# Optimization experiments

Hardware: AMD Instinct MI355X
Metric: run time of the kernel (lower is better)

## Reference

```python
import jax, jax.numpy as jnp
import numpy as np

N_HEAD = 16

def _alibi_slopes(num_heads):
    # m_i = (256 ** (1/num_heads)) ** -(i+1)
    x = (2.0 ** 8) ** (1.0 / num_heads)
    return jnp.asarray([1.0 / x ** (i + 1) for i in range(num_heads)], dtype=jnp.float32)

def setup_inputs() -> dict:
    key = jax.random.key(0)
    k1, k2 = jax.random.split(key)
    B, S, D = 2, 2048, 1024
    x = jax.random.normal(k1, (B, S, D), dtype=jnp.float32)
    W_kqv = jax.random.normal(k2, (D, 3 * D), dtype=jnp.float32) * 0.02
    return {"x": x, "W_kqv": W_kqv}

def reference(x, W_kqv):
    B, S, D = x.shape
    H = N_HEAD
    hd = D // H
    scale = jnp.sqrt(jnp.asarray(D, dtype=x.dtype))  # NOTE: sqrt(n_embd), per source
    kqv = x @ W_kqv                                   # [B,S,3D]
    k, q, v = jnp.split(kqv, 3, axis=-1)              # chunk order: key, query, value
    q = q.reshape(B, S, H, hd).transpose(0, 2, 1, 3)  # [B,H,S,hd]
    k = k.reshape(B, S, H, hd).transpose(0, 2, 1, 3)
    v = v.reshape(B, S, H, hd).transpose(0, 2, 1, 3)
    # ALiBi bias: m[h] * (j - i)
    pos = jnp.arange(S)
    rel = (pos[None, :] - pos[:, None]).astype(x.dtype)      # [S,S]
    m = _alibi_slopes(H).astype(x.dtype)                     # [H]
    bias = m[:, None, None] * rel                            # [H,S,S]
    score = jnp.einsum('bhqd,bhkd->bhqk', q, k) / scale + bias[None]
    causal = pos[None, :] <= pos[:, None]                    # [S,S] lower-tri
    score = jnp.where(causal[None, None], score, -jnp.inf)
    attn = jax.nn.softmax(score, axis=-1)                    # [B,H,S,S]
    out = jnp.einsum('bhqk,bhkd->bhqd', attn, v)
    out = out.transpose(0, 2, 1, 3).reshape(B, S, D)
    return (out, attn)
```

## Files before the change

kernel.cpp:

```cpp
#include <hip/hip_runtime.h>
#include <hip/hip_bf16.h>

typedef __attribute__((ext_vector_type(8))) short short8;
typedef __attribute__((ext_vector_type(4))) float f32x4;

static __device__ __forceinline__ unsigned short f2bf(float f) {
    unsigned int x = __float_as_uint(f);
    x += 0x7fffu + ((x >> 16) & 1u);
    return (unsigned short)(x >> 16);
}

static __device__ __forceinline__ void gld_lds16(const unsigned short* g, unsigned short* l) {
    __builtin_amdgcn_global_load_lds((const __attribute__((address_space(1))) void*)g,
                                     (__attribute__((address_space(3))) void*)l, 16, 0, 0);
}

__global__ __launch_bounds__(256) void cvt_x_kernel(const float* __restrict__ in,
                                                    unsigned short* __restrict__ outb,
                                                    int n4) {
    int i = blockIdx.x * 256 + threadIdx.x;
    if (i < n4) {
        f32x4 v = *(const f32x4*)(in + (size_t)i * 4);
        ushort4 o;
        o.x = f2bf(v[0]); o.y = f2bf(v[1]); o.z = f2bf(v[2]); o.w = f2bf(v[3]);
        *(ushort4*)(outb + (size_t)i * 4) = o;
    }
}

__global__ __launch_bounds__(256) void cvt_wt_kernel(const float* __restrict__ W,
                                                     unsigned short* __restrict__ WT) {
    __shared__ float t[64][65];
    const int n0 = blockIdx.x * 64;
    const int k0 = blockIdx.y * 64;
    const int tid = threadIdx.x;
#pragma unroll
    for (int i = 0; i < 16; ++i) {
        int lin = tid + i * 256;
        int rr = lin >> 6, cc = lin & 63;
        t[rr][cc] = W[(size_t)(k0 + rr) * 3072 + n0 + cc];
    }
    __syncthreads();
#pragma unroll
    for (int i = 0; i < 16; ++i) {
        int lin = tid + i * 256;
        int nn = lin >> 6, kk = lin & 63;
        WT[(size_t)(n0 + nn) * 1024 + k0 + kk] = f2bf(t[kk][nn]);
    }
}

__global__ __launch_bounds__(512, 2) void gemm_kqv_kernel(
    const unsigned short* __restrict__ A,
    const unsigned short* __restrict__ BT,
    unsigned short* __restrict__ qb,
    unsigned short* __restrict__ kb,
    unsigned short* __restrict__ vtb) {
    __shared__ __attribute__((aligned(16))) unsigned short smem[2 * 2 * 256 * 64];
    unsigned short (*As)[256][64] = (unsigned short(*)[256][64])smem;
    unsigned short (*Bs)[256][64] = (unsigned short(*)[256][64])(smem + 2 * 256 * 64);
    const int tid = threadIdx.x;
    const int w = tid >> 6, lane = tid & 63;
    const int quad = lane >> 4, cl = lane & 15;

    const int wg = (int)blockIdx.x + 12 * (int)blockIdx.y;
    const int wgs = (wg & 7) * 24 + (wg >> 3);
    const int m0 = (wgs / 12) * 256, n0 = (wgs % 12) * 256;
    const int wm = (w >> 2) * 128, wn = (w & 3) * 64;

    const int srow = lane >> 3;
    const int schk = (lane & 7) ^ srow;
    const unsigned short* Ap = A + (size_t)(m0 + w * 8 + srow) * 1024 + schk * 8;
    const unsigned short* Bp = BT + (size_t)(n0 + w * 8 + srow) * 1024 + schk * 8;

    f32x4 acc[8][4] = {};

    auto stageA = [&](int kk, int buf) {
#pragma unroll
        for (int i = 0; i < 4; ++i)
            gld_lds16(Ap + kk + (size_t)i * 64 * 1024, &As[buf][i * 64 + w * 8][0]);
    };
    auto stageB = [&](int kk, int buf) {
#pragma unroll
        for (int i = 0; i < 4; ++i)
            gld_lds16(Bp + kk + (size_t)i * 64 * 1024, &Bs[buf][i * 64 + w * 8][0]);
    };

    stageA(0, 0);
    stageB(0, 0);

    for (int kt = 0; kt < 16; ++kt) {
        const int cur = kt & 1;
        asm volatile("s_waitcnt vmcnt(0)" ::: "memory");
        __builtin_amdgcn_s_barrier();

        short8 bfr[4][2];
#pragma unroll
        for (int n = 0; n < 4; ++n)
#pragma unroll
            for (int kc = 0; kc < 2; ++kc)
                bfr[n][kc] = *(const short8*)
                    &Bs[cur][wn + n * 16 + cl][((kc * 4 + quad) ^ (cl & 7)) * 8];

#pragma unroll
        for (int q = 0; q < 4; ++q) {
            if (q == 0 && kt < 15) stageA(kt * 64 + 64, cur ^ 1);
            if (q == 1 && kt < 15) stageB(kt * 64 + 64, cur ^ 1);
            short8 af[2][2];
#pragma unroll
            for (int i = 0; i < 2; ++i)
#pragma unroll
                for (int kc = 0; kc < 2; ++kc)
                    af[i][kc] = *(const short8*)
                        &As[cur][wm + q * 32 + i * 16 + cl][((kc * 4 + quad) ^ (cl & 7)) * 8];
            __builtin_amdgcn_s_setprio(1);
#pragma unroll
            for (int i = 0; i < 2; ++i)
#pragma unroll
                for (int n = 0; n < 4; ++n)
#pragma unroll
                    for (int kc = 0; kc < 2; ++kc)
                        acc[q * 2 + i][n] = __builtin_amdgcn_mfma_f32_16x16x32_bf16(
                            af[i][kc], bfr[n][kc], acc[q * 2 + i][n], 0, 0, 0);
            __builtin_amdgcn_s_setprio(0);
            __builtin_amdgcn_sched_barrier(0);
            __builtin_amdgcn_s_barrier();
        }
    }

    const int chunk = n0 >> 10;
    const int d0 = n0 & 1023;
    const int b = m0 >> 11;
    const int s_base = m0 & 2047;

    if (chunk == 2) {
        unsigned short (*Cs)[256] = (unsigned short(*)[256])smem;
        __syncthreads();
#pragma unroll
        for (int im = 0; im < 8; ++im)
#pragma unroll
            for (int in = 0; in < 4; ++in)
#pragma unroll
                for (int rg = 0; rg < 4; ++rg) {
                    int dl = wn + in * 16 + cl;
                    int s = wm + im * 16 + quad * 4 + rg;
                    Cs[dl][(((s >> 3) ^ (dl & 7)) << 3) | (s & 7)] =
                        f2bf(acc[im][in][rg]);
                }
        __syncthreads();
#pragma unroll
        for (int it = 0; it < 16; ++it) {
            int l = it * 4096 + tid * 8;
            int dr = l >> 8;
            int r = l & 255;
            int d = d0 + dr, hh = d >> 6, dd = d & 63;
            size_t dst = ((size_t)(b * 16 + hh) * 64 + dd) * 2048 + s_base + r;
            *(uint4*)(vtb + dst) = *(const uint4*)&Cs[dr][(((r >> 3) ^ (dr & 7)) << 3)];
        }
    } else {
        unsigned short* outp = (chunk == 0) ? kb : qb;
#pragma unroll
        for (int im = 0; im < 8; ++im)
#pragma unroll
            for (int in = 0; in < 4; ++in)
#pragma unroll
                for (int rg = 0; rg < 4; ++rg) {
                    int s = s_base + wm + im * 16 + quad * 4 + rg;
                    int d = d0 + wn + in * 16 + cl;
                    int hh = d >> 6, dd = d & 63;
                    outp[((size_t)(b * 16 + hh) * 2048 + s) * 64 + dd] =
                        f2bf(acc[im][in][rg]);
                }
    }
}

__global__ __launch_bounds__(256, 2) void attn_kernel(
    const unsigned short* __restrict__ qb,
    const unsigned short* __restrict__ kb,
    const unsigned short* __restrict__ vtb,
    float* __restrict__ out_,
    float* __restrict__ attn) {
    const int h = blockIdx.y;
    const int b = blockIdx.z;
    const int bh = b * 16 + h;
    const int tid = threadIdx.x;
    const int w = tid >> 6;
    const int lane = tid & 63;
    const int quad = lane >> 4;
    const int cl = lane & 15;

    const unsigned short* Qh = qb + (size_t)bh * 2048 * 64;
    const unsigned short* Kh = kb + (size_t)bh * 2048 * 64;
    const unsigned short* Vh = vtb + (size_t)bh * 64 * 2048;
    float* attnh = attn + (size_t)bh * 2048 * 2048;

    __shared__ __attribute__((aligned(16))) unsigned short Kt[2][64][64];
    __shared__ __attribute__((aligned(16))) unsigned short Vt[2][64][64];
    __shared__ __attribute__((aligned(16))) unsigned short Ps[4][16][64];

    const int srow = lane >> 3;
    const int schk = (lane & 7) ^ srow;

    auto stageK = [&](int jt, int buf) {
#pragma unroll
        for (int i = 0; i < 2; ++i)
            gld_lds16(Kh + (size_t)(jt * 64 + w * 16 + i * 8 + srow) * 64 + schk * 8,
                      &Kt[buf][w * 16 + i * 8][0]);
    };
    auto stageV = [&](int j0, int buf) {
#pragma unroll
        for (int i = 0; i < 2; ++i)
            gld_lds16(Vh + (size_t)(w * 16 + i * 8 + srow) * 2048 + j0 + schk * 8,
                      &Vt[buf][w * 16 + i * 8][0]);
    };

    const float mh = exp2f(-0.5f * (float)(h + 1));
    const float sc1 = 1.0f / 32.0f;

    for (int half = 0; half < 2; ++half) {
        const int t64 = half ? 31 - (int)blockIdx.x : (int)blockIdx.x;
        const int q0 = t64 * 64;
        const int row0 = q0 + w * 16;
        const int jtmax = t64;

        short8 aq0 = *(const short8*)(Qh + (size_t)(row0 + cl) * 64 + quad * 8);
        short8 aq1 = *(const short8*)(Qh + (size_t)(row0 + cl) * 64 + 32 + quad * 8);

        float rsum[4] = {0.f, 0.f, 0.f, 0.f};
        __syncthreads();
        stageK(0, 0);
        {
            int cur = 0;
            for (int jt = 0; jt <= jtmax; ++jt, cur ^= 1) {
                __syncthreads();
                if (jt < jtmax) stageK(jt + 1, cur ^ 1);
                const int j0 = jt * 64;
#pragma unroll
                for (int nt = 0; nt < 4; ++nt) {
                    const int r = nt * 16 + cl;
                    short8 k0 = *(const short8*)&Kt[cur][r][((quad) ^ (cl & 7)) * 8];
                    short8 k1 = *(const short8*)&Kt[cur][r][((quad + 4) ^ (cl & 7)) * 8];
                    f32x4 s = {0.f, 0.f, 0.f, 0.f};
                    s = __builtin_amdgcn_mfma_f32_16x16x32_bf16(aq0, k0, s, 0, 0, 0);
                    s = __builtin_amdgcn_mfma_f32_16x16x32_bf16(aq1, k1, s, 0, 0, 0);
                    const int jc = j0 + nt * 16 + cl;
#pragma unroll
                    for (int rg = 0; rg < 4; ++rg) {
                        int irow = row0 + quad * 4 + rg;
                        if (jc <= irow)
                            rsum[rg] += __expf(s[rg] * sc1 + mh * (float)(jc - irow));
                    }
                }
            }
        }
#pragma unroll
        for (int rg = 0; rg < 4; ++rg) {
            float v = rsum[rg];
            v += __shfl_xor(v, 1);
            v += __shfl_xor(v, 2);
            v += __shfl_xor(v, 4);
            v += __shfl_xor(v, 8);
            rsum[rg] = 1.0f / v;
        }

        __syncthreads();
        f32x4 oacc[4] = {};
        stageK(0, 0);
        stageV(0, 0);
        {
            int cur = 0;
            for (int jt = 0; jt <= jtmax; ++jt, cur ^= 1) {
                __syncthreads();
                if (jt < jtmax) {
                    stageK(jt + 1, cur ^ 1);
                    stageV(jt * 64 + 64, cur ^ 1);
                }
                const int j0 = jt * 64;
                f32x4 sv[4];
#pragma unroll
                for (int nt = 0; nt < 4; ++nt) {
                    const int r = nt * 16 + cl;
                    short8 k0 = *(const short8*)&Kt[cur][r][((quad) ^ (cl & 7)) * 8];
                    short8 k1 = *(const short8*)&Kt[cur][r][((quad + 4) ^ (cl & 7)) * 8];
                    f32x4 s = {0.f, 0.f, 0.f, 0.f};
                    s = __builtin_amdgcn_mfma_f32_16x16x32_bf16(aq0, k0, s, 0, 0, 0);
                    sv[nt] = __builtin_amdgcn_mfma_f32_16x16x32_bf16(aq1, k1, s, 0, 0, 0);
                }
#pragma unroll
                for (int nt = 0; nt < 4; ++nt) {
                    const int jc = j0 + nt * 16 + cl;
#pragma unroll
                    for (int rg = 0; rg < 4; ++rg) {
                        const int irow = row0 + quad * 4 + rg;
                        float p = (jc <= irow)
                                      ? __expf(sv[nt][rg] * sc1 + mh * (float)(jc - irow)) * rsum[rg]
                                      : 0.f;
                        Ps[w][quad * 4 + rg]
                          [(((nt * 2 + (cl >> 3)) ^ ((quad * 4 + rg) & 7)) << 3) | (cl & 7)] =
                            f2bf(p);
                        __builtin_nontemporal_store(p, attnh + (size_t)irow * 2048 + jc);
                    }
                }

                short8 pa0 = *(const short8*)&Ps[w][cl][((quad ^ (cl & 7)) << 3)];
                short8 pa1 = *(const short8*)&Ps[w][cl][((((quad + 4)) ^ (cl & 7)) << 3)];

#pragma unroll
                for (int on = 0; on < 4; ++on) {
                    const int r = on * 16 + cl;
                    short8 v0 = *(const short8*)&Vt[cur][r][((quad) ^ (cl & 7)) * 8];
                    short8 v1 = *(const short8*)&Vt[cur][r][((quad + 4) ^ (cl & 7)) * 8];
                    oacc[on] = __builtin_amdgcn_mfma_f32_16x16x32_bf16(pa0, v0, oacc[on], 0, 0, 0);
                    oacc[on] = __builtin_amdgcn_mfma_f32_16x16x32_bf16(pa1, v1, oacc[on], 0, 0, 0);
                }
            }
        }

#pragma unroll
        for (int on = 0; on < 4; ++on) {
#pragma unroll
            for (int rg = 0; rg < 4; ++rg) {
                int srow2 = row0 + quad * 4 + rg;
                __builtin_nontemporal_store(
                    oacc[on][rg], out_ + ((size_t)b * 2048 + srow2) * 1024 + h * 64 + on * 16 + cl);
            }
        }

        const int jz = (jtmax + 1) * 64;
        if (jz < 2048) {
            f32x4 z = {0.f, 0.f, 0.f, 0.f};
            for (int rr = 0; rr < 16; ++rr) {
                float* dst = attnh + (size_t)(row0 + rr) * 2048;
                for (int c = jz + lane * 4; c < 2048; c += 256)
                    __builtin_nontemporal_store(z, (f32x4*)(dst + c));
            }
        }
    }
}

extern "C" void kernel_launch(void* const* d_in, const int* in_sizes, int n_in,
                              void* d_out, int out_size, void* d_ws, size_t ws_size,
                              hipStream_t stream) {
    const float* x = (const float*)d_in[0];
    const float* Wk = (const float*)d_in[1];
    float* out = (float*)d_out;
    float* attn = out + (size_t)2 * 2048 * 1024;

    unsigned short* xb = (unsigned short*)d_ws;
    unsigned short* wtb = xb + (size_t)4096 * 1024;
    unsigned short* qb = wtb + (size_t)3072 * 1024;
    unsigned short* kb = qb + (size_t)32 * 2048 * 64;
    unsigned short* vtb = kb + (size_t)32 * 2048 * 64;

    cvt_x_kernel<<<dim3(4096), dim3(256), 0, stream>>>(x, xb, 4096 * 1024 / 4);
    cvt_wt_kernel<<<dim3(48, 16), dim3(256), 0, stream>>>(Wk, wtb);
    gemm_kqv_kernel<<<dim3(12, 16), dim3(512), 0, stream>>>(xb, wtb, qb, kb, vtb);
    attn_kernel<<<dim3(16, 16, 2), dim3(256), 0, stream>>>(qb, kb, vtb, out, attn);
}
```

Before: 687.0 us.

## Stage two K/V tiles per barrier and coalesce K/Q projection stores via LDS

New measurement: 678.8 us. About the same (-1.2%).

```diff
diff --git a/kernel.cpp b/kernel.cpp
--- a/kernel.cpp
+++ b/kernel.cpp
@@ -157,18 +157,29 @@
         }
     } else {
         unsigned short* outp = (chunk == 0) ? kb : qb;
+        unsigned short (*Cs)[256] = (unsigned short(*)[256])smem;
+        __syncthreads();
 #pragma unroll
         for (int im = 0; im < 8; ++im)
 #pragma unroll
             for (int in = 0; in < 4; ++in)
 #pragma unroll
                 for (int rg = 0; rg < 4; ++rg) {
-                    int s = s_base + wm + im * 16 + quad * 4 + rg;
-                    int d = d0 + wn + in * 16 + cl;
-                    int hh = d >> 6, dd = d & 63;
-                    outp[((size_t)(b * 16 + hh) * 2048 + s) * 64 + dd] =
+                    int s = wm + im * 16 + quad * 4 + rg;
+                    int d = wn + in * 16 + cl;
+                    Cs[s][(((d >> 3) ^ (s & 7)) << 3) | (d & 7)] =
                         f2bf(acc[im][in][rg]);
                 }
+        __syncthreads();
+#pragma unroll
+        for (int it = 0; it < 16; ++it) {
+            int l = it * 4096 + tid * 8;
+            int sr = l >> 8;
+            int c = l & 255;
+            int d = d0 + c, hh = d >> 6, dd = d & 63;
+            size_t dst = ((size_t)(b * 16 + hh) * 2048 + s_base + sr) * 64 + dd;
+            *(uint4*)(outp + dst) = *(const uint4*)&Cs[sr][(((c >> 3) ^ (sr & 7)) << 3)];
+        }
     }
 }
 
@@ -192,24 +203,24 @@
     const unsigned short* Vh = vtb + (size_t)bh * 64 * 2048;
     float* attnh = attn + (size_t)bh * 2048 * 2048;
 
-    __shared__ __attribute__((aligned(16))) unsigned short Kt[2][64][64];
-    __shared__ __attribute__((aligned(16))) unsigned short Vt[2][64][64];
+    __shared__ __attribute__((aligned(16))) unsigned short Kt[2][2][64][64];
+    __shared__ __attribute__((aligned(16))) unsigned short Vt[2][2][64][64];
     __shared__ __attribute__((aligned(16))) unsigned short Ps[4][16][64];
 
     const int srow = lane >> 3;
     const int schk = (lane & 7) ^ srow;
 
-    auto stageK = [&](int jt, int buf) {
+    auto stageK = [&](int jt, int buf, int sub) {
 #pragma unroll
         for (int i = 0; i < 2; ++i)
             gld_lds16(Kh + (size_t)(jt * 64 + w * 16 + i * 8 + srow) * 64 + schk * 8,
-                      &Kt[buf][w * 16 + i * 8][0]);
+                      &Kt[buf][sub][w * 16 + i * 8][0]);
     };
-    auto stageV = [&](int j0, int buf) {
+    auto stageV = [&](int jt, int buf, int sub) {
 #pragma unroll
         for (int i = 0; i < 2; ++i)
-            gld_lds16(Vh + (size_t)(w * 16 + i * 8 + srow) * 2048 + j0 + schk * 8,
-                      &Vt[buf][w * 16 + i * 8][0]);
+            gld_lds16(Vh + (size_t)(w * 16 + i * 8 + srow) * 2048 + jt * 64 + schk * 8,
+                      &Vt[buf][sub][w * 16 + i * 8][0]);
     };
 
     const float mh = exp2f(-0.5f * (float)(h + 1));
@@ -220,33 +231,42 @@
         const int q0 = t64 * 64;
         const int row0 = q0 + w * 16;
         const int jtmax = t64;
+        const int N64 = jtmax + 1;
+        const int NS = (N64 + 1) >> 1;
 
         short8 aq0 = *(const short8*)(Qh + (size_t)(row0 + cl) * 64 + quad * 8);
         short8 aq1 = *(const short8*)(Qh + (size_t)(row0 + cl) * 64 + 32 + quad * 8);
 
         float rsum[4] = {0.f, 0.f, 0.f, 0.f};
         __syncthreads();
-        stageK(0, 0);
-        {
-            int cur = 0;
-            for (int jt = 0; jt <= jtmax; ++jt, cur ^= 1) {
-                __syncthreads();
-                if (jt < jtmax) stageK(jt + 1, cur ^ 1);
+        stageK(0, 0, 0);
+        if (1 < N64) stageK(1, 0, 1);
+        for (int s = 0; s < NS; ++s) {
+            const int cur = s & 1;
+            __syncthreads();
+            if (s + 1 < NS) {
+                stageK(2 * s + 2, cur ^ 1, 0);
+                if (2 * s + 3 < N64) stageK(2 * s + 3, cur ^ 1, 1);
+            }
+#pragma unroll
+            for (int sub = 0; sub < 2; ++sub) {
+                const int jt = 2 * s + sub;
+                if (jt >= N64) continue;
                 const int j0 = jt * 64;
 #pragma unroll
                 for (int nt = 0; nt < 4; ++nt) {
                     const int r = nt * 16 + cl;
-                    short8 k0 = *(const short8*)&Kt[cur][r][((quad) ^ (cl & 7)) * 8];
-                    short8 k1 = *(const short8*)&Kt[cur][r][((quad + 4) ^ (cl & 7)) * 8];
-                    f32x4 s = {0.f, 0.f, 0.f, 0.f};
-                    s = __builtin_amdgcn_mfma_f32_16x16x32_bf16(aq0, k0, s, 0, 0, 0);
-                    s = __builtin_amdgcn_mfma_f32_16x16x32_bf16(aq1, k1, s, 0, 0, 0);
+                    short8 k0 = *(const short8*)&Kt[cur][sub][r][((quad) ^ (cl & 7)) * 8];
+                    short8 k1 = *(const short8*)&Kt[cur][sub][r][((quad + 4) ^ (cl & 7)) * 8];
+                    f32x4 sx = {0.f, 0.f, 0.f, 0.f};
+                    sx = __builtin_amdgcn_mfma_f32_16x16x32_bf16(aq0, k0, sx, 0, 0, 0);
+                    sx = __builtin_amdgcn_mfma_f32_16x16x32_bf16(aq1, k1, sx, 0, 0, 0);
                     const int jc = j0 + nt * 16 + cl;
 #pragma unroll
                     for (int rg = 0; rg < 4; ++rg) {
                         int irow = row0 + quad * 4 + rg;
                         if (jc <= irow)
-                            rsum[rg] += __expf(s[rg] * sc1 + mh * (float)(jc - irow));
+                            rsum[rg] += __expf(sx[rg] * sc1 + mh * (float)(jc - irow));
                     }
                 }
             }
@@ -263,26 +283,34 @@
 
         __syncthreads();
         f32x4 oacc[4] = {};
-        stageK(0, 0);
-        stageV(0, 0);
-        {
-            int cur = 0;
-            for (int jt = 0; jt <= jtmax; ++jt, cur ^= 1) {
-                __syncthreads();
-                if (jt < jtmax) {
-                    stageK(jt + 1, cur ^ 1);
-                    stageV(jt * 64 + 64, cur ^ 1);
-                }
+        stageK(0, 0, 0);
+        stageV(0, 0, 0);
+        if (1 < N64) { stageK(1, 0, 1); stageV(1, 0, 1); }
+        for (int s = 0; s < NS; ++s) {
+            const int cur = s & 1;
+            __syncthreads();
+            if (s + 1 < NS) {
+                stageK(2 * s + 2, cur ^ 1, 0);
+                stageV(2 * s + 2, cur ^ 1, 0);
+                if (2 * s + 3 < N64) {
+                    stageK(2 * s + 3, cur ^ 1, 1);
+                    stageV(2 * s + 3, cur ^ 1, 1);
+                }
+            }
+#pragma unroll
+            for (int sub = 0; sub < 2; ++sub) {
+                const int jt = 2 * s + sub;
+                if (jt >= N64) continue;
                 const int j0 = jt * 64;
                 f32x4 sv[4];
 #pragma unroll
                 for (int nt = 0; nt < 4; ++nt) {
                     const int r = nt * 16 + cl;
-                    short8 k0 = *(const short8*)&Kt[cur][r][((quad) ^ (cl & 7)) * 8];
-                    short8 k1 = *(const short8*)&Kt[cur][r][((quad + 4) ^ (cl & 7)) * 8];
-                    f32x4 s = {0.f, 0.f, 0.f, 0.f};
-                    s = __builtin_amdgcn_mfma_f32_16x16x32_bf16(aq0, k0, s, 0, 0, 0);
-                    sv[nt] = __builtin_amdgcn_mfma_f32_16x16x32_bf16(aq1, k1, s, 0, 0, 0);
+                    short8 k0 = *(const short8*)&Kt[cur][sub][r][((quad) ^ (cl & 7)) * 8];
+                    short8 k1 = *(const short8*)&Kt[cur][sub][r][((quad + 4) ^ (cl & 7)) * 8];
+                    f32x4 sx = {0.f, 0.f, 0.f, 0.f};
+                    sx = __builtin_amdgcn_mfma_f32_16x16x32_bf16(aq0, k0, sx, 0, 0, 0);
+                    sv[nt] = __builtin_amdgcn_mfma_f32_16x16x32_bf16(aq1, k1, sx, 0, 0, 0);
                 }
 #pragma unroll
                 for (int nt = 0; nt < 4; ++nt) {
@@ -306,8 +334,8 @@
 #pragma unroll
                 for (int on = 0; on < 4; ++on) {
                     const int r = on * 16 + cl;
-                    short8 v0 = *(const short8*)&Vt[cur][r][((quad) ^ (cl & 7)) * 8];
-                    short8 v1 = *(const short8*)&Vt[cur][r][((quad + 4) ^ (cl & 7)) * 8];
+                    short8 v0 = *(const short8*)&Vt[cur][sub][r][((quad) ^ (cl & 7)) * 8];
+                    short8 v1 = *(const short8*)&Vt[cur][sub][r][((quad + 4) ^ (cl & 7)) * 8];
                     oacc[on] = __builtin_amdgcn_mfma_f32_16x16x32_bf16(pa0, v0, oacc[on], 0, 0, 0);
                     oacc[on] = __builtin_amdgcn_mfma_f32_16x16x32_bf16(pa1, v1, oacc[on], 0, 0, 0);
                 }
```
